# Kernel optimization log

Hardware: AMD Instinct MI355X
Metric: run time of the kernel (lower is better)

Reference implementation:

```python
import jax, jax.numpy as jnp
import numpy as np

B, S, D = 4, 2048, 1024
SCALE = float(np.sqrt(D))


def setup_inputs() -> dict:
    key = jax.random.key(0)
    ks = jax.random.split(key, 11)
    def lin(kw, kb):
        bound = 1.0 / np.sqrt(D)
        W = jax.random.uniform(kw, (D, D), jnp.float32, -bound, bound)
        b = jax.random.uniform(kb, (D,), jnp.float32, -bound, bound)
        return W, b
    wq, bq = lin(ks[0], ks[1])
    wk, bk = lin(ks[2], ks[3])
    wv, bv = lin(ks[4], ks[5])
    wo, bo = lin(ks[6], ks[7])
    q = jax.random.normal(ks[8], (B, S, D), jnp.float32)
    k = jax.random.normal(ks[9], (B, S, D), jnp.float32)
    v = jax.random.normal(ks[10], (B, S, D), jnp.float32)
    mask = jnp.tril(jnp.ones((S, S), jnp.int32))  # causal mask; 0 -> -inf
    return {"q": q, "k": k, "v": v, "mask": mask,
            "wq": wq, "bq": bq, "wk": wk, "bk": bk,
            "wv": wv, "bv": bv, "wo": wo, "bo": bo}


def reference(q, k, v, mask, wq, bq, wk, bk, wv, bv, wo, bo):
    # Linear layers: x @ W^T + b (torch convention with W stored [out,in];
    # here W is [D,D] uniform so we use x @ W + b equivalently)
    Q = q @ wq + bq            # [B,S,D]
    K = k @ wk + bk
    V = v @ wv + bv
    logits = jnp.einsum('bsd,btd->bst', Q, K) / SCALE  # [B,S,S]
    logits = jnp.where(mask == 0, -jnp.inf, logits)
    probs = jax.nn.softmax(logits, axis=-1)
    ctx = jnp.einsum('bst,btd->bsd', probs, V)
    return ctx @ wo + bo
```

## Files before the change

### kernel.cpp

```cpp
#include <hip/hip_runtime.h>
#include <hip/hip_bf16.h>
#include <cstdint>

using u16 = unsigned short;
typedef short s16x8 __attribute__((ext_vector_type(8)));
typedef short s16x4 __attribute__((ext_vector_type(4)));
typedef float f32x4 __attribute__((ext_vector_type(4)));

#define DI __device__ __forceinline__

DI u16 f2bf(float f) {
  union { float f; unsigned u; } x; x.f = f;
  unsigned r = x.u + 0x7fffu + ((x.u >> 16) & 1u);
  return (u16)(r >> 16);
}

DI s16x4 cvt4(float4 a) {
  s16x4 p;
  p[0] = (short)f2bf(a.x); p[1] = (short)f2bf(a.y);
  p[2] = (short)f2bf(a.z); p[3] = (short)f2bf(a.w);
  return p;
}

DI void gload_lds16(const u16* g, u16* l) {
  __builtin_amdgcn_global_load_lds((const __attribute__((address_space(1))) void*)g,
                                   (__attribute__((address_space(3))) void*)l,
                                   16, 0, 0);
}

template <int N> DI void vm_wait() {
  if constexpr (N == 0) asm volatile("s_waitcnt vmcnt(0)" ::: "memory");
  else if constexpr (N == 4) asm volatile("s_waitcnt vmcnt(4)" ::: "memory");
}
DI void lgkm0() { asm volatile("s_waitcnt lgkmcnt(0)" ::: "memory"); }

enum { M_PROJ = 0, M_QK = 1, M_PV = 2, M_OUT = 3 };

__global__ __launch_bounds__(256)
void cast3(const float* __restrict__ q, const float* __restrict__ k,
           const float* __restrict__ v, u16* __restrict__ qo,
           u16* __restrict__ ko, u16* __restrict__ vo, long n4) {
  const long stride = (long)gridDim.x * 256;
  for (long i = (long)blockIdx.x * 256 + threadIdx.x; i < n4; i += stride) {
    *(s16x4*)(qo + i * 4) = cvt4(((const float4*)q)[i]);
    *(s16x4*)(ko + i * 4) = cvt4(((const float4*)k)[i]);
    *(s16x4*)(vo + i * 4) = cvt4(((const float4*)v)[i]);
  }
}

template <int MODE>
__global__ __launch_bounds__(256, 2)
void gemm128(const u16* __restrict__ Ab, const u16* __restrict__ Btb,
             const float* __restrict__ b0, const float* __restrict__ b1,
             const float* __restrict__ b2, void* __restrict__ Cb,
             int N, int K, long sA, long sB, long sC, float scale)
{
  __shared__ __align__(16) char smem[69632];
  u16* AsBase = (u16*)smem;
  u16* BsBase = (u16*)(smem + 32768);

  const int tid  = threadIdx.x;
  const int lane = tid & 63;
  const int wid  = tid >> 6;
  const int wr   = wid >> 1, wc = wid & 1;
  const int l15  = lane & 15, l4 = lane >> 4;
  const int bz   = blockIdx.z;

  const int gx  = gridDim.x;
  const int nwg = gx * gridDim.y;
  const int hb  = blockIdx.y * gx + blockIdx.x;
  const int lb  = (hb & 7) * (nwg >> 3) + (hb >> 3);
  const int m0  = (lb / gx) * 128, n0 = (lb % gx) * 128;

  if constexpr (MODE == M_QK) {
    if (n0 > m0 + 127) return;
  }
  const int klim = (MODE == M_PV) ? min(K, m0 + 128) : K;
  const int nt = klim >> 6;

  const u16* A  = Ab  + (long)bz * sA;
  const u16* Bp = Btb + (long)bz * sB;

  auto STAGE_A = [&](int buf, int k0) {
    u16* dst = AsBase + buf * (128 * 64);
    #pragma unroll
    for (int it = 0; it < 4; ++it) {
      const int ct = it * 256 + tid;
      const int rl = ct >> 3, s = ct & 7;
      const int ss = s ^ (rl & 7);
      gload_lds16(A + (long)(m0 + rl) * K + (k0 + ss * 8), dst + rl * 64 + s * 8);
    }
  };
  auto STAGE_B = [&](int buf, int k0) {
    u16* dst = BsBase + buf * (128 * 64);
    #pragma unroll
    for (int it = 0; it < 4; ++it) {
      const int ct = it * 256 + tid;
      const int rl = ct >> 3, s = ct & 7;
      const int ss = s ^ (rl & 7);
      gload_lds16(Bp + (long)(n0 + rl) * K + (k0 + ss * 8), dst + rl * 64 + s * 8);
    }
  };

  f32x4 acc[4][4] = {};
  s16x8 afr[4], bfr[4];

  auto LOAD_FRAGS = [&](int buf, int ks) {
    const u16* ab = AsBase + buf * (128 * 64);
    const u16* bb = BsBase + buf * (128 * 64);
    #pragma unroll
    for (int i = 0; i < 4; ++i) {
      const int row = wr * 64 + i * 16 + l15;
      const int sl  = (ks * 4 + l4) ^ (row & 7);
      afr[i] = *(const s16x8*)(ab + row * 64 + sl * 8);
    }
    #pragma unroll
    for (int j = 0; j < 4; ++j) {
      const int row = wc * 64 + j * 16 + l15;
      const int sl  = (ks * 4 + l4) ^ (row & 7);
      bfr[j] = *(const s16x8*)(bb + row * 64 + sl * 8);
    }
  };
  auto MFMA16 = [&]() {
    __builtin_amdgcn_s_setprio(1);
    #pragma unroll
    for (int i = 0; i < 4; ++i)
      #pragma unroll
      for (int j = 0; j < 4; ++j)
        acc[i][j] = __builtin_amdgcn_mfma_f32_16x16x32_bf16(afr[i], bfr[j], acc[i][j], 0, 0, 0);
    __builtin_amdgcn_s_setprio(0);
  };

  STAGE_A(0, 0); STAGE_B(0, 0);
  int cur = 0;
  for (int t = 0; t < nt; ++t) {
    const int kn = (t + 1) << 6;
    const bool pf = (t + 1 < nt);
    if (pf) { STAGE_A(cur ^ 1, kn); vm_wait<4>(); }
    else    { vm_wait<0>(); }
    __builtin_amdgcn_sched_barrier(0);
    __builtin_amdgcn_s_barrier();
    LOAD_FRAGS(cur, 0);
    lgkm0(); __builtin_amdgcn_sched_barrier(0);
    MFMA16();
    __builtin_amdgcn_s_barrier();
    LOAD_FRAGS(cur, 1);
    if (pf) STAGE_B(cur ^ 1, kn);
    __builtin_amdgcn_s_barrier();
    lgkm0(); __builtin_amdgcn_sched_barrier(0);
    MFMA16();
    __builtin_amdgcn_s_barrier();
    cur ^= 1;
  }

  const int rb = m0 + wr * 64, cb = n0 + wc * 64;

  if constexpr (MODE == M_PROJ || MODE == M_PV) {
    const float* bias = (MODE == M_PROJ) ? (bz == 0 ? b0 : (bz == 1 ? b1 : b2)) : nullptr;
    u16* ep = (u16*)smem + (size_t)wid * (64 * 72);
    #pragma unroll
    for (int nj = 0; nj < 4; ++nj) {
      const float badd = (MODE == M_PROJ) ? bias[cb + nj * 16 + l15] : 0.f;
      #pragma unroll
      for (int mi = 0; mi < 4; ++mi)
        #pragma unroll
        for (int r = 0; r < 4; ++r)
          ep[(mi * 16 + l4 * 4 + r) * 72 + nj * 16 + l15] = f2bf(acc[mi][nj][r] + badd);
    }
    lgkm0();
    u16* C = (u16*)Cb + (long)bz * sC;
    #pragma unroll
    for (int it = 0; it < 8; ++it) {
      const int idx = it * 64 + lane;
      const int lr = idx >> 3, lc = (idx & 7) * 8;
      s16x8 vv = *(const s16x8*)(ep + lr * 72 + lc);
      *(s16x8*)&C[(long)(rb + lr) * N + cb + lc] = vv;
    }
  } else {
    float* ep = (float*)smem + (size_t)wid * (64 * 68);
    #pragma unroll
    for (int nj = 0; nj < 4; ++nj) {
      const float badd = (MODE == M_OUT) ? b0[cb + nj * 16 + l15] : 0.f;
      #pragma unroll
      for (int mi = 0; mi < 4; ++mi)
        #pragma unroll
        for (int r = 0; r < 4; ++r) {
          float val = acc[mi][nj][r];
          if constexpr (MODE == M_QK) val *= scale; else val += badd;
          ep[(mi * 16 + l4 * 4 + r) * 68 + nj * 16 + l15] = val;
        }
    }
    lgkm0();
    float* C = (float*)Cb + (long)bz * sC;
    #pragma unroll
    for (int it = 0; it < 16; ++it) {
      const int idx = it * 64 + lane;
      const int lr = idx >> 4, lc = (idx & 15) * 4;
      float4 vv = *(const float4*)(ep + lr * 68 + lc);
      *(float4*)&C[(long)(rb + lr) * N + cb + lc] = vv;
    }
  }
}

__global__ __launch_bounds__(256)
void transpose_v(const u16* __restrict__ in, u16* __restrict__ out, int R, int C) {
  __shared__ u16 t[32][33];
  const long bo = (long)blockIdx.z * R * C;
  const int r0 = blockIdx.y * 32, c0 = blockIdx.x * 32;
  const int tx = threadIdx.x & 31, ty = threadIdx.x >> 5;
  #pragma unroll
  for (int i = 0; i < 32; i += 8)
    t[ty + i][tx] = in[bo + (long)(r0 + ty + i) * C + (c0 + tx)];
  __syncthreads();
  #pragma unroll
  for (int i = 0; i < 32; i += 8)
    out[bo + (long)(c0 + ty + i) * R + (r0 + tx)] = t[tx][ty + i];
}

__global__ __launch_bounds__(256)
void prep_weights(const float* __restrict__ w0, const float* __restrict__ w1,
                  const float* __restrict__ w2, const float* __restrict__ w3,
                  u16* __restrict__ out, int D) {
  __shared__ float t[32][33];
  const int z = blockIdx.z;
  const float* W = (z == 0) ? w0 : (z == 1) ? w1 : (z == 2) ? w2 : w3;
  u16* o = out + (long)z * D * D;
  const int r0 = blockIdx.y * 32, c0 = blockIdx.x * 32;
  const int tx = threadIdx.x & 31, ty = threadIdx.x >> 5;
  #pragma unroll
  for (int i = 0; i < 32; i += 8)
    t[ty + i][tx] = W[(long)(r0 + ty + i) * D + (c0 + tx)];
  __syncthreads();
  #pragma unroll
  for (int i = 0; i < 32; i += 8)
    o[(long)(c0 + ty + i) * D + (r0 + tx)] = f2bf(t[tx][ty + i]);
}

__global__ __launch_bounds__(256)
void softmax_causal(const float* __restrict__ logits, u16* __restrict__ probs, int S) {
  const int s = blockIdx.x, b = blockIdx.y;
  const float* row = logits + ((long)b * S + s) * S;
  u16* orow = probs + ((long)b * S + s) * S;
  const int n = s + 1;
  const int n4 = n >> 2;
  const int jmax = (n + 127) & ~127;
  const int tid = threadIdx.x, lane = tid & 63, w = tid >> 6;
  const float4* row4 = (const float4*)row;
  __shared__ float red[8];

  float m = -1e30f;
  for (int i = tid; i < n4; i += 256) {
    float4 t = row4[i];
    m = fmaxf(m, fmaxf(fmaxf(t.x, t.y), fmaxf(t.z, t.w)));
  }
  for (int j = (n4 << 2) + tid; j < n; j += 256) m = fmaxf(m, row[j]);
  #pragma unroll
  for (int off = 32; off > 0; off >>= 1) m = fmaxf(m, __shfl_xor(m, off));
  if (lane == 0) red[w] = m;
  __syncthreads();
  m = fmaxf(fmaxf(red[0], red[1]), fmaxf(red[2], red[3]));

  float ssum = 0.f;
  for (int i = tid; i < n4; i += 256) {
    float4 t = row4[i];
    ssum += __expf(t.x - m) + __expf(t.y - m) + __expf(t.z - m) + __expf(t.w - m);
  }
  for (int j = (n4 << 2) + tid; j < n; j += 256) ssum += __expf(row[j] - m);
  #pragma unroll
  for (int off = 32; off > 0; off >>= 1) ssum += __shfl_xor(ssum, off);
  if (lane == 0) red[4 + w] = ssum;
  __syncthreads();
  const float inv = 1.f / (red[4] + red[5] + red[6] + red[7]);

  for (int i = tid; i < (jmax >> 2); i += 256) {
    float4 t = row4[i];
    const int j = i << 2;
    s16x4 p;
    p[0] = (short)((j + 0 < n) ? f2bf(__expf(t.x - m) * inv) : 0);
    p[1] = (short)((j + 1 < n) ? f2bf(__expf(t.y - m) * inv) : 0);
    p[2] = (short)((j + 2 < n) ? f2bf(__expf(t.z - m) * inv) : 0);
    p[3] = (short)((j + 3 < n) ? f2bf(__expf(t.w - m) * inv) : 0);
    *(s16x4*)(orow + j) = p;
  }
}

extern "C" void kernel_launch(void* const* d_in, const int* in_sizes, int n_in,
                              void* d_out, int out_size, void* d_ws, size_t ws_size,
                              hipStream_t stream)
{
  constexpr int B = 4, S = 2048, D = 1024;
  constexpr long DD = (long)D * D;
  const float* q  = (const float*)d_in[0];
  const float* k  = (const float*)d_in[1];
  const float* v  = (const float*)d_in[2];
  const float* wq = (const float*)d_in[4];
  const float* bq = (const float*)d_in[5];
  const float* wk = (const float*)d_in[6];
  const float* bk = (const float*)d_in[7];
  const float* wv = (const float*)d_in[8];
  const float* bv = (const float*)d_in[9];
  const float* wo = (const float*)d_in[10];
  const float* bo = (const float*)d_in[11];

  char* ws = (char*)d_ws;
  const long MB = 1024 * 1024;
  u16*   wt     = (u16*)(ws + 0 * MB);
  u16*   Qb     = (u16*)(ws + 8 * MB);
  u16*   Kb     = (u16*)(ws + 24 * MB);
  u16*   Vb     = (u16*)(ws + 40 * MB);
  u16*   Vt     = (u16*)(ws + 56 * MB);
  float* logits = (float*)(ws + 72 * MB);
  u16*   qc     = (u16*)(ws + 136 * MB);
  u16*   kc     = (u16*)(ws + 152 * MB);
  u16*   vc     = (u16*)(ws + 168 * MB);
  u16*   probs  = (u16*)(ws + 136 * MB);
  u16*   ctx    = (u16*)(ws + 168 * MB);

  constexpr long PSTRIDE = 8L * 1024 * 1024;

  const dim3 b256(256);
  cast3<<<2048, b256, 0, stream>>>(q, k, v, qc, kc, vc, (long)B * S * D / 4);
  prep_weights<<<dim3(32, 32, 4), b256, 0, stream>>>(wq, wk, wv, wo, wt, D);
  gemm128<M_PROJ><<<dim3(8, 64, 3), b256, 0, stream>>>(
      qc, wt, bq, bk, bv, Qb, D, D, PSTRIDE, DD, PSTRIDE, 1.f);
  transpose_v<<<dim3(32, 64, 4), b256, 0, stream>>>(Vb, Vt, S, D);
  gemm128<M_QK><<<dim3(16, 16, 4), b256, 0, stream>>>(
      Qb, Kb, nullptr, nullptr, nullptr, logits, S, D,
      (long)S * D, (long)S * D, (long)S * S, 1.f / 32.f);
  softmax_causal<<<dim3(S, B), b256, 0, stream>>>(logits, probs, S);
  gemm128<M_PV><<<dim3(8, 16, 4), b256, 0, stream>>>(
      probs, Vt, nullptr, nullptr, nullptr, ctx, D, S,
      (long)S * S, (long)D * S, (long)S * D, 1.f);
  gemm128<M_OUT><<<dim3(8, 64, 1), b256, 0, stream>>>(
      ctx, wt + 3 * DD, bo, nullptr, nullptr, d_out, D, D, 0, 0, 0, 1.f);
}
```

Baseline: 336.5 us.

## Fuse softmax into QK epilogue and PV prologue, fuse V transpose into projection

The QK GEMM epilogue now emits per-row, per-64-column partial max and sum-of-exp values. A small reduce_ml kernel combines these into a row max and inverse sum. A new gemm_pv kernel loads fp32 logits directly, applies exp, normalisation and the causal mask in registers, and writes bf16 into LDS, so the separate softmax pass and the probs buffer go away. The V projection epilogue writes V already transposed, which removes the transpose kernel. The trade-off is that the PV kernel now reads fp32 logits, twice the bytes of bf16 probs, and does exp work inside the GEMM loop, which may stall the MFMA pipeline.

```diff
diff --git a/kernel.cpp b/kernel.cpp
--- a/kernel.cpp
+++ b/kernel.cpp
@@ -31,10 +31,11 @@
 template <int N> DI void vm_wait() {
   if constexpr (N == 0) asm volatile("s_waitcnt vmcnt(0)" ::: "memory");
   else if constexpr (N == 4) asm volatile("s_waitcnt vmcnt(4)" ::: "memory");
+  else if constexpr (N == 12) asm volatile("s_waitcnt vmcnt(12)" ::: "memory");
 }
 DI void lgkm0() { asm volatile("s_waitcnt lgkmcnt(0)" ::: "memory"); }
 
-enum { M_PROJ = 0, M_QK = 1, M_PV = 2, M_OUT = 3 };
+enum { M_PROJ = 0, M_QK = 1, M_OUT = 3 };
 
 __global__ __launch_bounds__(256)
 void cast3(const float* __restrict__ q, const float* __restrict__ k,
@@ -53,6 +54,7 @@
 void gemm128(const u16* __restrict__ Ab, const u16* __restrict__ Btb,
              const float* __restrict__ b0, const float* __restrict__ b1,
              const float* __restrict__ b2, void* __restrict__ Cb,
+             float2* __restrict__ part, u16* __restrict__ vtp,
              int N, int K, long sA, long sB, long sC, float scale)
 {
   __shared__ __align__(16) char smem[69632];
@@ -75,8 +77,7 @@
   if constexpr (MODE == M_QK) {
     if (n0 > m0 + 127) return;
   }
-  const int klim = (MODE == M_PV) ? min(K, m0 + 128) : K;
-  const int nt = klim >> 6;
+  const int nt = K >> 6;
 
   const u16* A  = Ab  + (long)bz * sA;
   const u16* Bp = Btb + (long)bz * sB;
@@ -155,66 +156,270 @@
 
   const int rb = m0 + wr * 64, cb = n0 + wc * 64;
 
-  if constexpr (MODE == M_PROJ || MODE == M_PV) {
-    const float* bias = (MODE == M_PROJ) ? (bz == 0 ? b0 : (bz == 1 ? b1 : b2)) : nullptr;
-    u16* ep = (u16*)smem + (size_t)wid * (64 * 72);
-    #pragma unroll
-    for (int nj = 0; nj < 4; ++nj) {
-      const float badd = (MODE == M_PROJ) ? bias[cb + nj * 16 + l15] : 0.f;
+  if constexpr (MODE == M_PROJ) {
+    const float* bias = (bz == 0) ? b0 : (bz == 1 ? b1 : b2);
+    if (bz == 2) {
+      u16* ep = (u16*)smem + (size_t)wid * (64 * 72);
+      #pragma unroll
+      for (int nj = 0; nj < 4; ++nj) {
+        const float badd = bias[cb + nj * 16 + l15];
+        #pragma unroll
+        for (int mi = 0; mi < 4; ++mi)
+          #pragma unroll
+          for (int r = 0; r < 4; ++r)
+            ep[(nj * 16 + l15) * 72 + mi * 16 + l4 * 4 + r] = f2bf(acc[mi][nj][r] + badd);
+      }
+      lgkm0();
+      const int batch = rb >> 11, scol = rb & 2047;
+      u16* Vt = vtp + (long)batch * (1024 * 2048);
+      #pragma unroll
+      for (int it = 0; it < 8; ++it) {
+        const int idx = it * 64 + lane;
+        const int dr = idx >> 3, sc = (idx & 7) * 8;
+        *(s16x8*)&Vt[(long)(cb + dr) * 2048 + scol + sc] = *(const s16x8*)(ep + dr * 72 + sc);
+      }
+    } else {
+      u16* ep = (u16*)smem + (size_t)wid * (64 * 72);
+      #pragma unroll
+      for (int nj = 0; nj < 4; ++nj) {
+        const float badd = bias[cb + nj * 16 + l15];
+        #pragma unroll
+        for (int mi = 0; mi < 4; ++mi)
+          #pragma unroll
+          for (int r = 0; r < 4; ++r)
+            ep[(mi * 16 + l4 * 4 + r) * 72 + nj * 16 + l15] = f2bf(acc[mi][nj][r] + badd);
+      }
+      lgkm0();
+      u16* C = (u16*)Cb + (long)bz * sC;
+      #pragma unroll
+      for (int it = 0; it < 8; ++it) {
+        const int idx = it * 64 + lane;
+        const int lr = idx >> 3, lc = (idx & 7) * 8;
+        *(s16x8*)&C[(long)(rb + lr) * N + cb + lc] = *(const s16x8*)(ep + lr * 72 + lc);
+      }
+    }
+  } else if constexpr (MODE == M_QK) {
+    {
+      const int chunk = cb >> 6;
+      #pragma unroll
+      for (int mi = 0; mi < 4; ++mi)
+        #pragma unroll
+        for (int r = 0; r < 4; ++r) {
+          const int grow = rb + mi * 16 + l4 * 4 + r;
+          float vs[4];
+          float vmax = -3e38f;
+          #pragma unroll
+          for (int nj = 0; nj < 4; ++nj) {
+            float x = acc[mi][nj][r] * scale;
+            x = ((cb + nj * 16 + l15) <= grow) ? x : -3e38f;
+            vs[nj] = x;
+            vmax = fmaxf(vmax, x);
+          }
+          #pragma unroll
+          for (int d = 1; d < 16; d <<= 1) vmax = fmaxf(vmax, __shfl_xor(vmax, d));
+          float ss = 0.f;
+          #pragma unroll
+          for (int nj = 0; nj < 4; ++nj) ss += __expf(vs[nj] - vmax);
+          #pragma unroll
+          for (int d = 1; d < 16; d <<= 1) ss += __shfl_xor(ss, d);
+          if (l15 == 0)
+            part[((long)bz * 2048 + grow) * 32 + chunk] = make_float2(vmax, ss);
+        }
+    }
+    float* ep = (float*)smem + (size_t)wid * (64 * 68);
+    #pragma unroll
+    for (int nj = 0; nj < 4; ++nj)
       #pragma unroll
       for (int mi = 0; mi < 4; ++mi)
         #pragma unroll
         for (int r = 0; r < 4; ++r)
-          ep[(mi * 16 + l4 * 4 + r) * 72 + nj * 16 + l15] = f2bf(acc[mi][nj][r] + badd);
-    }
-    lgkm0();
-    u16* C = (u16*)Cb + (long)bz * sC;
-    #pragma unroll
-    for (int it = 0; it < 8; ++it) {
-      const int idx = it * 64 + lane;
-      const int lr = idx >> 3, lc = (idx & 7) * 8;
-      s16x8 vv = *(const s16x8*)(ep + lr * 72 + lc);
-      *(s16x8*)&C[(long)(rb + lr) * N + cb + lc] = vv;
-    }
-  } else {
-    float* ep = (float*)smem + (size_t)wid * (64 * 68);
-    #pragma unroll
-    for (int nj = 0; nj < 4; ++nj) {
-      const float badd = (MODE == M_OUT) ? b0[cb + nj * 16 + l15] : 0.f;
-      #pragma unroll
-      for (int mi = 0; mi < 4; ++mi)
-        #pragma unroll
-        for (int r = 0; r < 4; ++r) {
-          float val = acc[mi][nj][r];
-          if constexpr (MODE == M_QK) val *= scale; else val += badd;
-          ep[(mi * 16 + l4 * 4 + r) * 68 + nj * 16 + l15] = val;
-        }
-    }
+          ep[(mi * 16 + l4 * 4 + r) * 68 + nj * 16 + l15] = acc[mi][nj][r] * scale;
     lgkm0();
     float* C = (float*)Cb + (long)bz * sC;
     #pragma unroll
     for (int it = 0; it < 16; ++it) {
       const int idx = it * 64 + lane;
       const int lr = idx >> 4, lc = (idx & 15) * 4;
-      float4 vv = *(const float4*)(ep + lr * 68 + lc);
-      *(float4*)&C[(long)(rb + lr) * N + cb + lc] = vv;
+      *(float4*)&C[(long)(rb + lr) * N + cb + lc] = *(const float4*)(ep + lr * 68 + lc);
+    }
+  } else {
+    float* ep = (float*)smem + (size_t)wid * (64 * 68);
+    #pragma unroll
+    for (int nj = 0; nj < 4; ++nj) {
+      const float badd = b0[cb + nj * 16 + l15];
+      #pragma unroll
+      for (int mi = 0; mi < 4; ++mi)
+        #pragma unroll
+        for (int r = 0; r < 4; ++r)
+          ep[(mi * 16 + l4 * 4 + r) * 68 + nj * 16 + l15] = acc[mi][nj][r] + badd;
+    }
+    lgkm0();
+    float* C = (float*)Cb;
+    #pragma unroll
+    for (int it = 0; it < 16; ++it) {
+      const int idx = it * 64 + lane;
+      const int lr = idx >> 4, lc = (idx & 15) * 4;
+      *(float4*)&C[(long)(rb + lr) * N + cb + lc] = *(const float4*)(ep + lr * 68 + lc);
     }
   }
 }
 
 __global__ __launch_bounds__(256)
-void transpose_v(const u16* __restrict__ in, u16* __restrict__ out, int R, int C) {
-  __shared__ u16 t[32][33];
-  const long bo = (long)blockIdx.z * R * C;
-  const int r0 = blockIdx.y * 32, c0 = blockIdx.x * 32;
-  const int tx = threadIdx.x & 31, ty = threadIdx.x >> 5;
+void reduce_ml(const float2* __restrict__ part, float2* __restrict__ ml) {
+  const int gid = blockIdx.x * 256 + threadIdx.x;
+  const int row = gid & 2047;
+  const float2* p = part + (long)gid * 32;
+  const int nc = (row >> 6) + 1;
+  float m = -3e38f;
+  for (int c = 0; c < nc; ++c) m = fmaxf(m, p[c].x);
+  float l = 0.f;
+  for (int c = 0; c < nc; ++c) l += p[c].y * __expf(p[c].x - m);
+  ml[gid] = make_float2(m, 1.f / l);
+}
+
+__global__ __launch_bounds__(256, 2)
+void gemm_pv(const float* __restrict__ logits, const u16* __restrict__ Vtb,
+             const float2* __restrict__ ml, u16* __restrict__ ctx)
+{
+  constexpr int S = 2048, D = 1024;
+  __shared__ __align__(16) char smem[69632];
+  u16* AsBase = (u16*)smem;
+  u16* BsBase = (u16*)(smem + 32768);
+
+  const int tid  = threadIdx.x;
+  const int lane = tid & 63;
+  const int wid  = tid >> 6;
+  const int wr   = wid >> 1, wc = wid & 1;
+  const int l15  = lane & 15, l4 = lane >> 4;
+  const int bz   = blockIdx.z;
+
+  const int gx  = gridDim.x;
+  const int nwg = gx * gridDim.y;
+  const int hb  = blockIdx.y * gx + blockIdx.x;
+  const int lb  = (hb & 7) * (nwg >> 3) + (hb >> 3);
+  const int m0  = (lb / gx) * 128, n0 = (lb % gx) * 128;
+
+  const int klim = m0 + 128;
+  const int nt = klim >> 6;
+
+  const float* A = logits + (long)bz * S * S;
+  const u16* Bp  = Vtb + (long)bz * (long)D * S;
+
+  float2 mlv[4];
   #pragma unroll
-  for (int i = 0; i < 32; i += 8)
-    t[ty + i][tx] = in[bo + (long)(r0 + ty + i) * C + (c0 + tx)];
-  __syncthreads();
+  for (int it = 0; it < 4; ++it) {
+    const int rl = (it * 256 + tid) >> 3;
+    mlv[it] = ml[bz * 2048 + m0 + rl];
+  }
+
+  float4 ar[8];
+  auto ALOAD = [&](int k0) {
+    #pragma unroll
+    for (int it = 0; it < 4; ++it) {
+      const int ct = it * 256 + tid;
+      const int rl = ct >> 3, s = ct & 7, ss = s ^ (rl & 7);
+      const float* src = A + (long)(m0 + rl) * S + k0 + ss * 8;
+      ar[it * 2]     = *(const float4*)src;
+      ar[it * 2 + 1] = *(const float4*)(src + 4);
+    }
+  };
+  auto ACONV = [&](int buf, int k0) {
+    u16* dst = AsBase + buf * (128 * 64);
+    #pragma unroll
+    for (int it = 0; it < 4; ++it) {
+      const int ct = it * 256 + tid;
+      const int rl = ct >> 3, s = ct & 7, ss = s ^ (rl & 7);
+      const int srow = m0 + rl, c0 = k0 + ss * 8;
+      const float mr = mlv[it].x, iv = mlv[it].y;
+      s16x8 p;
+      #pragma unroll
+      for (int e = 0; e < 8; ++e) {
+        const float x = (e < 4) ? ((const float*)&ar[it * 2])[e]
+                                : ((const float*)&ar[it * 2 + 1])[e - 4];
+        const float pe = __expf(x - mr) * iv;
+        p[e] = (short)((c0 + e <= srow) ? f2bf(pe) : (u16)0);
+      }
+      *(s16x8*)(dst + rl * 64 + s * 8) = p;
+    }
+  };
+  auto BSTAGE = [&](int buf, int k0) {
+    u16* dst = BsBase + buf * (128 * 64);
+    #pragma unroll
+    for (int it = 0; it < 4; ++it) {
+      const int ct = it * 256 + tid;
+      const int rl = ct >> 3, s = ct & 7, ss = s ^ (rl & 7);
+      gload_lds16(Bp + (long)(n0 + rl) * S + (k0 + ss * 8), dst + rl * 64 + s * 8);
+    }
+  };
+
+  f32x4 acc[4][4] = {};
+  s16x8 afr[4], bfr[4];
+  auto LOAD_FRAGS = [&](int buf, int ks) {
+    const u16* ab = AsBase + buf * (128 * 64);
+    const u16* bb = BsBase + buf * (128 * 64);
+    #pragma unroll
+    for (int i = 0; i < 4; ++i) {
+      const int row = wr * 64 + i * 16 + l15;
+      const int sl  = (ks * 4 + l4) ^ (row & 7);
+      afr[i] = *(const s16x8*)(ab + row * 64 + sl * 8);
+    }
+    #pragma unroll
+    for (int j = 0; j < 4; ++j) {
+      const int row = wc * 64 + j * 16 + l15;
+      const int sl  = (ks * 4 + l4) ^ (row & 7);
+      bfr[j] = *(const s16x8*)(bb + row * 64 + sl * 8);
+    }
+  };
+  auto MFMA16 = [&]() {
+    __builtin_amdgcn_s_setprio(1);
+    #pragma unroll
+    for (int i = 0; i < 4; ++i)
+      #pragma unroll
+      for (int j = 0; j < 4; ++j)
+        acc[i][j] = __builtin_amdgcn_mfma_f32_16x16x32_bf16(afr[i], bfr[j], acc[i][j], 0, 0, 0);
+    __builtin_amdgcn_s_setprio(0);
+  };
+
+  ALOAD(0); BSTAGE(0, 0);
+  ACONV(0, 0);
+  lgkm0();
+  int cur = 0;
+  for (int t = 0; t < nt; ++t) {
+    const int kn = (t + 1) << 6;
+    const bool pf = (t + 1 < nt);
+    if (pf) { ALOAD(kn); BSTAGE(cur ^ 1, kn); }
+    __builtin_amdgcn_sched_barrier(0);
+    if (pf) vm_wait<12>(); else vm_wait<0>();
+    __builtin_amdgcn_s_barrier();
+    LOAD_FRAGS(cur, 0);
+    lgkm0(); __builtin_amdgcn_sched_barrier(0);
+    MFMA16();
+    LOAD_FRAGS(cur, 1);
+    lgkm0(); __builtin_amdgcn_sched_barrier(0);
+    MFMA16();
+    if (pf) ACONV(cur ^ 1, kn);
+    lgkm0();
+    __builtin_amdgcn_s_barrier();
+    cur ^= 1;
+  }
+
+  const int rb = m0 + wr * 64, cb = n0 + wc * 64;
+  u16* ep = (u16*)smem + (size_t)wid * (64 * 72);
   #pragma unroll
-  for (int i = 0; i < 32; i += 8)
-    out[bo + (long)(c0 + ty + i) * R + (r0 + tx)] = t[tx][ty + i];
+  for (int nj = 0; nj < 4; ++nj)
+    #pragma unroll
+    for (int mi = 0; mi < 4; ++mi)
+      #pragma unroll
+      for (int r = 0; r < 4; ++r)
+        ep[(mi * 16 + l4 * 4 + r) * 72 + nj * 16 + l15] = f2bf(acc[mi][nj][r]);
+  lgkm0();
+  u16* C = ctx + (long)bz * S * D;
+  #pragma unroll
+  for (int it = 0; it < 8; ++it) {
+    const int idx = it * 64 + lane;
+    const int lr = idx >> 3, lc = (idx & 7) * 8;
+    *(s16x8*)&C[(long)(rb + lr) * D + cb + lc] = *(const s16x8*)(ep + lr * 72 + lc);
+  }
 }
 
 __global__ __launch_bounds__(256)
@@ -236,54 +441,6 @@
     o[(long)(c0 + ty + i) * D + (r0 + tx)] = f2bf(t[tx][ty + i]);
 }
 
-__global__ __launch_bounds__(256)
-void softmax_causal(const float* __restrict__ logits, u16* __restrict__ probs, int S) {
-  const int s = blockIdx.x, b = blockIdx.y;
-  const float* row = logits + ((long)b * S + s) * S;
-  u16* orow = probs + ((long)b * S + s) * S;
-  const int n = s + 1;
-  const int n4 = n >> 2;
-  const int jmax = (n + 127) & ~127;
-  const int tid = threadIdx.x, lane = tid & 63, w = tid >> 6;
-  const float4* row4 = (const float4*)row;
-  __shared__ float red[8];
-
-  float m = -1e30f;
-  for (int i = tid; i < n4; i += 256) {
-    float4 t = row4[i];
-    m = fmaxf(m, fmaxf(fmaxf(t.x, t.y), fmaxf(t.z, t.w)));
-  }
-  for (int j = (n4 << 2) + tid; j < n; j += 256) m = fmaxf(m, row[j]);
-  #pragma unroll
-  for (int off = 32; off > 0; off >>= 1) m = fmaxf(m, __shfl_xor(m, off));
-  if (lane == 0) red[w] = m;
-  __syncthreads();
-  m = fmaxf(fmaxf(red[0], red[1]), fmaxf(red[2], red[3]));
-
-  float ssum = 0.f;
-  for (int i = tid; i < n4; i += 256) {
-    float4 t = row4[i];
-    ssum += __expf(t.x - m) + __expf(t.y - m) + __expf(t.z - m) + __expf(t.w - m);
-  }
-  for (int j = (n4 << 2) + tid; j < n; j += 256) ssum += __expf(row[j] - m);
-  #pragma unroll
-  for (int off = 32; off > 0; off >>= 1) ssum += __shfl_xor(ssum, off);
-  if (lane == 0) red[4 + w] = ssum;
-  __syncthreads();
-  const float inv = 1.f / (red[4] + red[5] + red[6] + red[7]);
-
-  for (int i = tid; i < (jmax >> 2); i += 256) {
-    float4 t = row4[i];
-    const int j = i << 2;
-    s16x4 p;
-    p[0] = (short)((j + 0 < n) ? f2bf(__expf(t.x - m) * inv) : 0);
-    p[1] = (short)((j + 1 < n) ? f2bf(__expf(t.y - m) * inv) : 0);
-    p[2] = (short)((j + 2 < n) ? f2bf(__expf(t.z - m) * inv) : 0);
-    p[3] = (short)((j + 3 < n) ? f2bf(__expf(t.w - m) * inv) : 0);
-    *(s16x4*)(orow + j) = p;
-  }
-}
-
 extern "C" void kernel_launch(void* const* d_in, const int* in_sizes, int n_in,
                               void* d_out, int out_size, void* d_ws, size_t ws_size,
                               hipStream_t stream)
@@ -304,17 +461,17 @@
 
   char* ws = (char*)d_ws;
   const long MB = 1024 * 1024;
-  u16*   wt     = (u16*)(ws + 0 * MB);
-  u16*   Qb     = (u16*)(ws + 8 * MB);
-  u16*   Kb     = (u16*)(ws + 24 * MB);
-  u16*   Vb     = (u16*)(ws + 40 * MB);
-  u16*   Vt     = (u16*)(ws + 56 * MB);
-  float* logits = (float*)(ws + 72 * MB);
-  u16*   qc     = (u16*)(ws + 136 * MB);
-  u16*   kc     = (u16*)(ws + 152 * MB);
-  u16*   vc     = (u16*)(ws + 168 * MB);
-  u16*   probs  = (u16*)(ws + 136 * MB);
-  u16*   ctx    = (u16*)(ws + 168 * MB);
+  u16*    wt     = (u16*)(ws + 0 * MB);
+  u16*    Qb     = (u16*)(ws + 8 * MB);
+  u16*    Kb     = (u16*)(ws + 24 * MB);
+  u16*    Vt     = (u16*)(ws + 40 * MB);
+  float*  logits = (float*)(ws + 56 * MB);
+  float2* part   = (float2*)(ws + 120 * MB);
+  float2* ml     = (float2*)(ws + 122 * MB);
+  u16*    qc     = (u16*)(ws + 124 * MB);
+  u16*    kc     = (u16*)(ws + 140 * MB);
+  u16*    vc     = (u16*)(ws + 156 * MB);
+  u16*    ctx    = (u16*)(ws + 124 * MB);
 
   constexpr long PSTRIDE = 8L * 1024 * 1024;
 
@@ -322,15 +479,13 @@
   cast3<<<2048, b256, 0, stream>>>(q, k, v, qc, kc, vc, (long)B * S * D / 4);
   prep_weights<<<dim3(32, 32, 4), b256, 0, stream>>>(wq, wk, wv, wo, wt, D);
   gemm128<M_PROJ><<<dim3(8, 64, 3), b256, 0, stream>>>(
-      qc, wt, bq, bk, bv, Qb, D, D, PSTRIDE, DD, PSTRIDE, 1.f);
-  transpose_v<<<dim3(32, 64, 4), b256, 0, stream>>>(Vb, Vt, S, D);
+      qc, wt, bq, bk, bv, Qb, nullptr, Vt, D, D, PSTRIDE, DD, PSTRIDE, 1.f);
   gemm128<M_QK><<<dim3(16, 16, 4), b256, 0, stream>>>(
-      Qb, Kb, nullptr, nullptr, nullptr, logits, S, D,
+      Qb, Kb, nullptr, nullptr, nullptr, logits, part, nullptr, S, D,
       (long)S * D, (long)S * D, (long)S * S, 1.f / 32.f);
-  softmax_causal<<<dim3(S, B), b256, 0, stream>>>(logits, probs, S);
-  gemm128<M_PV><<<dim3(8, 16, 4), b256, 0, stream>>>(
-      probs, Vt, nullptr, nullptr, nullptr, ctx, D, S,
-      (long)S * S, (long)D * S, (long)S * D, 1.f);
+  reduce_ml<<<32, b256, 0, stream>>>(part, ml);
+  gemm_pv<<<dim3(8, 16, 4), b256, 0, stream>>>(logits, Vt, ml, ctx);
   gemm128<M_OUT><<<dim3(8, 64, 1), b256, 0, stream>>>(
-      ctx, wt + 3 * DD, bo, nullptr, nullptr, d_out, D, D, 0, 0, 0, 1.f);
-}
+      ctx, wt + 3 * DD, bo, nullptr, nullptr, d_out, nullptr, nullptr,
+      D, D, 0, 0, 0, 1.f);
+}
```

New measurement: 391.4 us. 16.3% more time.
